# Kernel optimization log

Measured on AMD Instinct MI355X. Metric: run time of the kernel, lower is better.

The kernel has to match this reference:

```python
import jax, jax.numpy as jnp
import numpy as np


def _conv(x, w, b, stride=1, pad=0):
    # x: NCHW, w: OIHW
    y = jax.lax.conv_general_dilated(
        x, w, (stride, stride), [(pad, pad), (pad, pad)],
        dimension_numbers=('NCHW', 'OIHW', 'NCHW'))
    return y + b[None, :, None, None]


def _upsample2x(x):
    b, c, h, w = x.shape
    return jax.image.resize(x, (b, c, 2 * h, 2 * w), method='bilinear')


def setup_inputs() -> dict:
    key = jax.random.key(0)
    ks = jax.random.split(key, 16)
    B, H, W = 32, 256, 256
    K, D = 512, 64  # codebook_dim, latent_dim

    def kaiming(k, shape, fan_in):
        return jax.random.normal(k, shape, jnp.float32) * np.sqrt(2.0 / fan_in)

    inp = {
        'x': jax.random.uniform(ks[0], (B, 3, H, W), jnp.float32),
        'codebook': kaiming(ks[1], (K, D), D),
        'enc_w1': kaiming(ks[2], (64, 3, 3, 3), 3 * 9),
        'enc_b1': jnp.zeros((64,), jnp.float32),
        'enc_w2': kaiming(ks[3], (32, 64, 3, 3), 64 * 9),
        'enc_b2': jnp.zeros((32,), jnp.float32),
        'enc_w3': kaiming(ks[4], (D, 32, 1, 1), 32),
        'enc_b3': jnp.zeros((D,), jnp.float32),
        'dec_w1': kaiming(ks[5], (32, D, 1, 1), D),
        'dec_b1': jnp.zeros((32,), jnp.float32),
        'dec_w2': kaiming(ks[6], (64, 32, 3, 3), 32 * 9),
        'dec_b2': jnp.zeros((64,), jnp.float32),
        'dec_w3': kaiming(ks[7], (3, 64, 3, 3), 64 * 9),
        'dec_b3': jnp.zeros((3,), jnp.float32),
    }
    return inp


def reference(x, codebook, enc_w1, enc_b1, enc_w2, enc_b2, enc_w3, enc_b3,
              dec_w1, dec_b1, dec_w2, dec_b2, dec_w3, dec_b3):
    # ---- encoder ----
    h = jax.nn.relu(_conv(x, enc_w1, enc_b1, stride=2, pad=1))
    h = jax.nn.relu(_conv(h, enc_w2, enc_b2, stride=2, pad=1))
    latent = _conv(h, enc_w3, enc_b3)  # [B, D, h, w]

    b, c, hh, ww = latent.shape
    z = latent.transpose(0, 2, 3, 1).reshape(-1, c)  # [(b h w), D]

    # squared Euclidean distances; argmin identical to cdist argmin
    d2 = (jnp.sum(z * z, axis=1, keepdims=True)
          - 2.0 * z @ codebook.T
          + jnp.sum(codebook * codebook, axis=1)[None, :])
    indices = jnp.argmin(d2, axis=1)
    zq = codebook[indices]  # [(b h w), D]

    codebook_loss = jnp.mean((zq - jax.lax.stop_gradient(z)) ** 2)
    commitment_loss = jnp.mean((jax.lax.stop_gradient(zq) - z) ** 2)

    # straight-through estimator
    zq = z + jax.lax.stop_gradient(zq - z)
    zq = zq.reshape(b, hh, ww, c).transpose(0, 3, 1, 2)  # [B, D, h, w]

    # ---- decoder ----
    d = jax.nn.relu(_conv(zq, dec_w1, dec_b1))
    d = _upsample2x(d)
    d = jax.nn.relu(_conv(d, dec_w2, dec_b2, pad=1))
    d = _upsample2x(d)
    recon = _conv(d, dec_w3, dec_b3, pad=1)

    return codebook_loss, commitment_loss, recon
```

## Files before the change

kernel.cpp:

```cpp
#include <hip/hip_runtime.h>
#include <hip/hip_bf16.h>

static constexpr int Bn = 32;
static constexpr int Hin = 256, Win = 256;
static constexpr int C1 = 64, H1 = 128, W1 = 128;
static constexpr int C2 = 32, H2 = 64, W2 = 64;
static constexpr int Dd = 64;
static constexpr int Kc = 512;
static constexpr int ROWS = Bn * H2 * W2;

static constexpr int K2A_FLOATS = 64 * 32 * 36;
static constexpr int K2B_FLOATS = 3 * 64 * 36;
static constexpr int T1_FLOATS  = Kc * C2;
static constexpr int G_FLOATS   = Kc * 9 * 64 * 4;
static constexpr int FIX_FLOATS = 64 + ROWS + 2 * ROWS + K2A_FLOATS +
                                  K2B_FLOATS + T1_FLOATS + G_FLOATS + 64;
static constexpr int H1_PER_N = C1 * H1 * W1;
static constexpr int Z_PER_N  = H2 * W2 * Dd;
static constexpr int H2_PER_N = C2 * H2 * W2;

__global__ __launch_bounds__(256) void k_init(
    float* __restrict__ lossA, unsigned long long* __restrict__ pk)
{
  int i = blockIdx.x * 256 + threadIdx.x;
  if (i < 64) lossA[i] = 0.f;
  pk[i] = 0xFFFFFFFFFFFFFFFFull;
}

__global__ __launch_bounds__(256) void k_wtrans(
    const float* __restrict__ w, float* __restrict__ k2, int N)
{
  int i = blockIdx.x * 256 + threadIdx.x;
  if (i >= N) return;
  float W[3][3];
#pragma unroll
  for (int ty = 0; ty < 3; ++ty)
#pragma unroll
    for (int tx = 0; tx < 3; ++tx) W[ty][tx] = w[i * 9 + ty * 3 + tx];
  const float A[2][3][3] = {
      {{.75f, .25f, 0.f}, {.25f, .75f, 0.f}, {0.f, .75f, .25f}},
      {{.25f, .75f, 0.f}, {0.f, .75f, .25f}, {0.f, .25f, .75f}}};
#pragma unroll
  for (int py = 0; py < 2; ++py)
#pragma unroll
    for (int px = 0; px < 2; ++px)
#pragma unroll
      for (int a = 0; a < 3; ++a)
#pragma unroll
        for (int b = 0; b < 3; ++b) {
          float v = 0.f;
#pragma unroll
          for (int ty = 0; ty < 3; ++ty)
#pragma unroll
            for (int tx = 0; tx < 3; ++tx)
              v += W[ty][tx] * A[py][ty][a] * A[px][tx][b];
          k2[(size_t)i * 36 + (py * 2 + px) * 9 + a * 3 + b] = v;
        }
}

__global__ __launch_bounds__(256) void k_gtab1(
    const float* __restrict__ cb, const float* __restrict__ w1,
    const float* __restrict__ b1, float* __restrict__ T1)
{
  int g = blockIdx.x * 256 + threadIdx.x;
  int e = g >> 5, ci = g & 31;
  const float* c = cb + e * Dd;
  const float* wr = w1 + ci * Dd;
  float a = 0.f;
#pragma unroll
  for (int d = 0; d < Dd; ++d) a += c[d] * wr[d];
  a += b1[ci];
  T1[g] = a > 0.f ? a : 0.f;
}

__global__ __launch_bounds__(256) void k_gtab2(
    const float* __restrict__ k2a, const float* __restrict__ T1,
    float* __restrict__ G)
{
  int e = blockIdx.x;
  int tid = threadIdx.x;
  int co = tid >> 2, ph = tid & 3;
  __shared__ float sT[32];
  if (tid < 32) sT[tid] = T1[e * 32 + tid];
  __syncthreads();
  float acc[9];
#pragma unroll
  for (int ab = 0; ab < 9; ++ab) acc[ab] = 0.f;
  for (int ci = 0; ci < 32; ++ci) {
    float tv = sT[ci];
    const float* kp = k2a + (size_t)(co * 32 + ci) * 36 + ph * 9;
#pragma unroll
    for (int ab = 0; ab < 9; ++ab) acc[ab] += tv * kp[ab];
  }
#pragma unroll
  for (int ab = 0; ab < 9; ++ab)
    G[((size_t)e * 9 + ab) * 256 + tid] = acc[ab];
}

__global__ __launch_bounds__(256) void k_conv1(
    const float* __restrict__ x, const float* __restrict__ w,
    const float* __restrict__ b, float* __restrict__ h1, int n0)
{
  int bid = blockIdx.x;
  int xt = bid & 1, yt = (bid >> 1) & 15, cc = (bid >> 5) & 3, n = bid >> 7;
  int X0 = xt * 64, Y0 = yt * 8, co0 = cc * 16;
  __shared__ float sIn[3][17][130];
  int tid = threadIdx.x;
  for (int i = tid; i < 3 * 17 * 130; i += 256) {
    int ci = i / (17 * 130);
    int rr = (i / 130) % 17;
    int ccx = i % 130;
    int gy = 2 * Y0 - 1 + rr, gx = 2 * X0 - 1 + ccx;
    float v = 0.f;
    if (gy >= 0 && gy < Hin && gx >= 0 && gx < Win)
      v = x[(((size_t)(n0 + n) * 3 + ci) * Hin + gy) * Win + gx];
    sIn[ci][rr][ccx] = v;
  }
  __syncthreads();
  int lx = tid & 63, ys = tid >> 6;
  float acc[16][2];
#pragma unroll
  for (int c = 0; c < 16; ++c) { acc[c][0] = 0.f; acc[c][1] = 0.f; }
#pragma unroll
  for (int ci = 0; ci < 3; ++ci)
#pragma unroll
    for (int ky = 0; ky < 3; ++ky)
#pragma unroll
      for (int kx = 0; kx < 3; ++kx) {
        float u0 = sIn[ci][2 * ys + ky][2 * lx + kx];
        float u1 = sIn[ci][2 * ys + 8 + ky][2 * lx + kx];
#pragma unroll
        for (int c = 0; c < 16; ++c) {
          float wv = w[((co0 + c) * 3 + ci) * 9 + ky * 3 + kx];
          acc[c][0] += u0 * wv;
          acc[c][1] += u1 * wv;
        }
      }
#pragma unroll
  for (int c = 0; c < 16; ++c) {
    float bv = b[co0 + c];
    float v0 = acc[c][0] + bv; v0 = v0 > 0.f ? v0 : 0.f;
    float v1 = acc[c][1] + bv; v1 = v1 > 0.f ? v1 : 0.f;
    h1[((n * C1 + co0 + c) * H1 + Y0 + ys) * W1 + X0 + lx] = v0;
    h1[((n * C1 + co0 + c) * H1 + Y0 + ys + 4) * W1 + X0 + lx] = v1;
  }
}

__global__ __launch_bounds__(256) void k_conv2(
    const float* __restrict__ h1, const float* __restrict__ w,
    const float* __restrict__ b, float* __restrict__ h2)
{
  int bid = blockIdx.x;
  int yt = bid & 15, cg = (bid >> 4) & 3, n = bid >> 6;
  int Y0 = yt * 4, co0 = cg * 8;
  __shared__ float sIn[4][9][132];
  int tid = threadIdx.x;
  int lane = tid & 63, ys = tid >> 6;
  float acc[8];
#pragma unroll
  for (int c = 0; c < 8; ++c) acc[c] = 0.f;
  for (int cb0 = 0; cb0 < C1; cb0 += 4) {
    __syncthreads();
    {
      const float* src = h1 + ((size_t)(n * C1 + cb0 + ys)) * (H1 * W1);
      float va[9], vb[9], vt[9];
#pragma unroll
      for (int rr = 0; rr < 9; ++rr) {
        int gy = 2 * Y0 - 1 + rr;
        bool yok = (gy >= 0) & (gy < H1);
        const float* rowp = src + gy * W1;
        va[rr] = (yok && lane > 0) ? rowp[lane - 1] : 0.f;
        vb[rr] = yok ? rowp[lane + 63] : 0.f;
        vt[rr] = (yok && lane == 0) ? rowp[127] : 0.f;
      }
      float* dst = &sIn[ys][0][0];
#pragma unroll
      for (int rr = 0; rr < 9; ++rr) {
        dst[rr * 132 + lane] = va[rr];
        dst[rr * 132 + 64 + lane] = vb[rr];
        if (lane < 2) dst[rr * 132 + 128 + lane] = (lane == 0) ? vt[rr] : 0.f;
      }
    }
    __syncthreads();
#pragma unroll
    for (int ci = 0; ci < 4; ++ci)
#pragma unroll
      for (int ky = 0; ky < 3; ++ky)
#pragma unroll
        for (int kx = 0; kx < 3; ++kx) {
          float u0 = sIn[ci][2 * ys + ky][2 * lane + kx];
#pragma unroll
          for (int c = 0; c < 8; ++c) {
            float wv = w[((co0 + c) * C1 + cb0 + ci) * 9 + ky * 3 + kx];
            acc[c] += u0 * wv;
          }
        }
  }
#pragma unroll
  for (int c = 0; c < 8; ++c) {
    float bv = b[co0 + c];
    float v0 = acc[c] + bv; v0 = v0 > 0.f ? v0 : 0.f;
    h2[((n * C2 + co0 + c) * H2 + Y0 + ys) * W2 + lane] = v0;
  }
}

__global__ __launch_bounds__(256) void k_conv3z(
    const float* __restrict__ h2, const float* __restrict__ w,
    const float* __restrict__ b, float* __restrict__ z)
{
  int bid = blockIdx.x;
  int y = bid & 63, n = bid >> 6;
  __shared__ float sH[C2][64];
  __shared__ float sW[Dd * 33];
  int tid = threadIdx.x;
  for (int i = tid; i < C2 * 64; i += 256) {
    int ci = i >> 6, xx = i & 63;
    sH[ci][xx] = h2[((n * C2 + ci) * H2 + y) * W2 + xx];
  }
  for (int i = tid; i < Dd * C2; i += 256) {
    int d = i >> 5, ci = i & 31;
    sW[d * 33 + ci] = w[i];
  }
  __syncthreads();
  int dg = tid & 3, lx = tid >> 2;
  float acc[16];
#pragma unroll
  for (int j = 0; j < 16; ++j) acc[j] = 0.f;
  for (int ci = 0; ci < C2; ++ci) {
    float u = sH[ci][lx];
#pragma unroll
    for (int j = 0; j < 16; ++j)
      acc[j] += u * sW[(dg * 16 + j) * 33 + ci];
  }
  int row = (n * H2 + y) * W2 + lx;
#pragma unroll
  for (int j = 0; j < 16; ++j)
    z[row * Dd + dg * 16 + j] = acc[j] + b[dg * 16 + j];
}

__global__ __launch_bounds__(256, 1) void k_vq(
    const float* __restrict__ z, const float* __restrict__ cbf,
    unsigned long long* __restrict__ pk, int row0)
{
  __shared__ float c2s[128];
  int bid = blockIdx.x;
  int sp = bid & 3, rb = bid >> 2;
  int c0 = sp * 128;
  int tid = threadIdx.x;
  if (tid < 128) {
    const float* cr = cbf + (size_t)(c0 + tid) * Dd;
    float s = 0.f;
#pragma unroll
    for (int d = 0; d < Dd; ++d) { float v = cr[d]; s += v * v; }
    c2s[tid] = s;
  }
  __syncthreads();
  int r = rb * 256 + tid;
  const float4* zp = (const float4*)(z + (size_t)r * Dd);
  float4 z0 = zp[0],  z1 = zp[1],  z2 = zp[2],  z3 = zp[3];
  float4 z4 = zp[4],  z5 = zp[5],  z6 = zp[6],  z7 = zp[7];
  float4 z8 = zp[8],  z9 = zp[9],  z10 = zp[10], z11 = zp[11];
  float4 z12 = zp[12], z13 = zp[13], z14 = zp[14], z15 = zp[15];
  float best = 1e30f; int bidx = c0;
#pragma unroll 2
  for (int c = 0; c < 128; ++c) {
    const float* __restrict__ cr = cbf + (size_t)(c0 + c) * Dd;
    float d0 = 0.f, d1 = 0.f, d2a = 0.f, d3 = 0.f;
#define VQ_DOT(ZV, K)                       \
    d0 = __builtin_fmaf(ZV.x, cr[4*K+0], d0); \
    d1 = __builtin_fmaf(ZV.y, cr[4*K+1], d1); \
    d2a = __builtin_fmaf(ZV.z, cr[4*K+2], d2a); \
    d3 = __builtin_fmaf(ZV.w, cr[4*K+3], d3);
    VQ_DOT(z0, 0)  VQ_DOT(z1, 1)  VQ_DOT(z2, 2)  VQ_DOT(z3, 3)
    VQ_DOT(z4, 4)  VQ_DOT(z5, 5)  VQ_DOT(z6, 6)  VQ_DOT(z7, 7)
    VQ_DOT(z8, 8)  VQ_DOT(z9, 9)  VQ_DOT(z10, 10) VQ_DOT(z11, 11)
    VQ_DOT(z12, 12) VQ_DOT(z13, 13) VQ_DOT(z14, 14) VQ_DOT(z15, 15)
#undef VQ_DOT
    float dot = (d0 + d1) + (d2a + d3);
    float dist = c2s[c] - 2.f * dot;
    if (dist < best) { best = dist; bidx = c0 + c; }
  }
  unsigned int u = __float_as_uint(best);
  unsigned int key32 = (u & 0x80000000u) ? ~u : (u | 0x80000000u);
  unsigned long long key =
      ((unsigned long long)key32 << 32) | (unsigned int)bidx;
  atomicMin(&pk[row0 + r], key);
}

__global__ __launch_bounds__(256) void k_vqfin(
    const float* __restrict__ z, const float* __restrict__ cbf,
    const unsigned long long* __restrict__ pk, int* __restrict__ idx,
    float* __restrict__ lossA, int row0)
{
  int r = blockIdx.x * 256 + threadIdx.x;
  int gi = row0 + r;
  int bidx = (int)(pk[gi] & 0xFFFFFFFFull);
  idx[gi] = bidx;
  const float4* zp = (const float4*)(z + (size_t)r * Dd);
  const float4* cr = (const float4*)(cbf + (size_t)bidx * Dd);
  float ls = 0.f;
#pragma unroll
  for (int i = 0; i < 16; ++i) {
    float4 zv = zp[i], cv = cr[i];
    float e0 = zv.x - cv.x, e1 = zv.y - cv.y;
    float e2 = zv.z - cv.z, e3 = zv.w - cv.w;
    ls += e0 * e0 + e1 * e1 + e2 * e2 + e3 * e3;
  }
#pragma unroll
  for (int off = 32; off > 0; off >>= 1) ls += __shfl_down(ls, off);
  if ((threadIdx.x & 63) == 0) atomicAdd(lossA, ls);
}

__global__ void k_loss_final(const float* __restrict__ a, float* __restrict__ out)
{
  if (threadIdx.x == 0) {
    float l = a[0] / (float)(ROWS * Dd);
    out[0] = l;
    out[1] = l;
  }
}

__global__ __launch_bounds__(256) void k_upg(
    const int* __restrict__ idx, const float* __restrict__ G,
    const float* __restrict__ bias, float* __restrict__ O, int row0)
{
  int bid = blockIdx.x;
  int tx = bid & 3; bid >>= 2;
  int ty = bid & 3; bid >>= 2;
  int cog = bid & 7; bid >>= 3;
  int n = bid;
  int Y0 = ty * 16, X0 = tx * 16, co0 = cog * 8;
  __shared__ int sIdx[18 * 18];
  int tid = threadIdx.x;
  int base = row0 + (n << 12);
  for (int i = tid; i < 324; i += 256) {
    int r = i / 18, c = i % 18;
    int gy = Y0 - 1 + r; gy = gy < 0 ? 0 : (gy > 63 ? 63 : gy);
    int gx = X0 - 1 + c; gx = gx < 0 ? 0 : (gx > 63 ? 63 : gx);
    sIdx[i] = idx[base + gy * 64 + gx];
  }
  __syncthreads();
  int xx = tid & 15, yy = tid >> 4;
  float4 acc[8];
#pragma unroll
  for (int j = 0; j < 8; ++j) acc[j] = make_float4(0.f, 0.f, 0.f, 0.f);
#pragma unroll
  for (int a = 0; a < 3; ++a)
#pragma unroll
    for (int b = 0; b < 3; ++b) {
      int e = sIdx[(yy + a) * 18 + xx + b];
      const float4* gp =
          (const float4*)(G + ((size_t)(e * 9 + a * 3 + b) * 256) + co0 * 4);
#pragma unroll
      for (int j = 0; j < 8; ++j) {
        float4 gv = gp[j];
        acc[j].x += gv.x; acc[j].y += gv.y;
        acc[j].z += gv.z; acc[j].w += gv.w;
      }
    }
  int oy = 2 * (Y0 + yy), ox = 2 * (X0 + xx);
#pragma unroll
  for (int j = 0; j < 8; ++j) {
    int co = co0 + j;
    float bv = bias[co];
    float2 r0, r1;
    r0.x = acc[j].x + bv; r0.y = acc[j].y + bv;
    r1.x = acc[j].z + bv; r1.y = acc[j].w + bv;
    r0.x = r0.x > 0.f ? r0.x : 0.f; r0.y = r0.y > 0.f ? r0.y : 0.f;
    r1.x = r1.x > 0.f ? r1.x : 0.f; r1.y = r1.y > 0.f ? r1.y : 0.f;
    size_t o = ((size_t)(n * 64 + co) * 128 + oy) * 128 + ox;
    *(float2*)&O[o] = r0;
    *(float2*)&O[o + 128] = r1;
  }
}

__global__ __launch_bounds__(256) void k_border_a(
    const int* __restrict__ idx, const float* __restrict__ T1,
    const float* __restrict__ w2, const float* __restrict__ b2,
    float* __restrict__ d2, int row0)
{
  int bid = blockIdx.x;
  int ch = bid & 1; bid >>= 1;
  int side = bid & 3; bid >>= 2;
  int n = bid;
  bool hside = side < 2;
  int rbase = (side == 1) ? 62 : 0;
  int cbase = (side == 3) ? 62 : 0;
  __shared__ int sE[128];
  __shared__ float sD[32 * 128];
  int tid = threadIdx.x;
  if (tid < 128) {
    int yy, xx;
    if (hside) { yy = rbase + (tid >> 6); xx = tid & 63; }
    else       { yy = tid >> 1; xx = cbase + (tid & 1); }
    sE[tid] = idx[row0 + (n << 12) + yy * 64 + xx];
  }
  __syncthreads();
  for (int t = tid; t < 32 * 128; t += 256) {
    int ci = t >> 7, j = t & 127;
    sD[t] = T1[sE[j] * 32 + ci];
  }
  __syncthreads();
  int px = tid & 127, q = tid >> 7;
  int co0 = (ch * 2 + q) * 16;
  int u, v;
  if (side == 0)      { u = 0;   v = px; }
  else if (side == 1) { u = 127; v = px; }
  else if (side == 2) { u = px;  v = 0;   if (px == 0 || px == 127) return; }
  else                { u = px;  v = 127; if (px == 0 || px == 127) return; }
  float acc[16];
#pragma unroll
  for (int j = 0; j < 16; ++j) acc[j] = 0.f;
  for (int ci = 0; ci < 32; ++ci) {
    const float* P = sD + ci * 128;
    float u9[9];
#pragma unroll
    for (int dy = -1; dy <= 1; ++dy)
#pragma unroll
      for (int dx = -1; dx <= 1; ++dx) {
        int uy = u + dy, ux = v + dx;
        float val = 0.f;
        if (uy >= 0 && uy < 128 && ux >= 0 && ux < 128) {
          int ky0, ky1, kx0, kx1; float ay0, ax0;
          if (uy & 1) { ky0 = uy >> 1; ky1 = ky0 + 1; ay0 = .75f; }
          else        { ky1 = uy >> 1; ky0 = ky1 - 1; ay0 = .25f; }
          if (ux & 1) { kx0 = ux >> 1; kx1 = kx0 + 1; ax0 = .75f; }
          else        { kx1 = ux >> 1; kx0 = kx1 - 1; ax0 = .25f; }
          ky0 = ky0 < 0 ? 0 : (ky0 > 63 ? 63 : ky0);
          ky1 = ky1 < 0 ? 0 : (ky1 > 63 ? 63 : ky1);
          kx0 = kx0 < 0 ? 0 : (kx0 > 63 ? 63 : kx0);
          kx1 = kx1 < 0 ? 0 : (kx1 > 63 ? 63 : kx1);
          int i00, i01, i10, i11;
          if (hside) {
            i00 = (ky0 - rbase) * 64 + kx0; i01 = (ky0 - rbase) * 64 + kx1;
            i10 = (ky1 - rbase) * 64 + kx0; i11 = (ky1 - rbase) * 64 + kx1;
          } else {
            i00 = ky0 * 2 + (kx0 - cbase); i01 = ky0 * 2 + (kx1 - cbase);
            i10 = ky1 * 2 + (kx0 - cbase); i11 = ky1 * 2 + (kx1 - cbase);
          }
          float ay1 = 1.f - ay0, ax1 = 1.f - ax0;
          val = ay0 * (ax0 * P[i00] + ax1 * P[i01]) +
                ay1 * (ax0 * P[i10] + ax1 * P[i11]);
        }
        u9[(dy + 1) * 3 + (dx + 1)] = val;
      }
#pragma unroll
    for (int j = 0; j < 16; ++j) {
      const float* wp = w2 + ((size_t)((co0 + j) * 32 + ci)) * 9;
#pragma unroll
      for (int tp = 0; tp < 9; ++tp) acc[j] += u9[tp] * wp[tp];
    }
  }
#pragma unroll
  for (int j = 0; j < 16; ++j) {
    int co = co0 + j;
    float val = acc[j] + b2[co];
    val = val > 0.f ? val : 0.f;
    d2[((size_t)(n * 64 + co) * 128 + u) * 128 + v] = val;
  }
}

__global__ __launch_bounds__(128) void k_upconv2x_b(
    const float* __restrict__ I, const float* __restrict__ k2,
    const float* __restrict__ bias, float* __restrict__ O, int n0)
{
  constexpr int Hi = 128, Ci = 64, Co = 3;
  int bid = blockIdx.x;
  int tx = bid & 3; bid >>= 2;
  int ty = bid & 15; bid >>= 4;
  int n = bid;
  int Y0 = ty * 8, X0 = tx * 32;
  __shared__ float sI[4][10 * 35];
  int tid = threadIdx.x;
  int lx = tid & 15, ly = tid >> 4;
  float4 acc[3][2];
#pragma unroll
  for (int j = 0; j < 3; ++j)
#pragma unroll
    for (int py = 0; py < 2; ++py) acc[j][py] = make_float4(0.f, 0.f, 0.f, 0.f);
  for (int c0 = 0; c0 < Ci; c0 += 4) {
    __syncthreads();
    for (int i = tid; i < 4 * 10 * 34; i += 128) {
      int s = i / 340, r2 = i % 340;
      int rr = r2 / 34, cc2 = r2 % 34;
      int gy = Y0 - 1 + rr; gy = gy < 0 ? 0 : (gy > Hi - 1 ? Hi - 1 : gy);
      int gx = X0 - 1 + cc2; gx = gx < 0 ? 0 : (gx > Hi - 1 ? Hi - 1 : gx);
      sI[s][rr * 35 + cc2] = I[((size_t)n * Ci + c0 + s) * Hi * Hi + gy * Hi + gx];
    }
    __syncthreads();
#pragma unroll
    for (int s = 0; s < 4; ++s) {
      float t[3][4];
#pragma unroll
      for (int r = 0; r < 3; ++r)
#pragma unroll
        for (int c = 0; c < 4; ++c)
          t[r][c] = sI[s][(ly + r) * 35 + 2 * lx + c];
#pragma unroll
      for (int j = 0; j < 3; ++j) {
        const float* kj = k2 + ((size_t)j * Ci + c0 + s) * 36;
#pragma unroll
        for (int a = 0; a < 3; ++a)
#pragma unroll
          for (int b = 0; b < 3; ++b) {
            float w00 = kj[a * 3 + b];
            float w01 = kj[9 + a * 3 + b];
            float w10 = kj[18 + a * 3 + b];
            float w11 = kj[27 + a * 3 + b];
            float i0 = t[a][b];
            float i1 = t[a][b + 1];
            acc[j][0].x += i0 * w00;
            acc[j][0].y += i0 * w01;
            acc[j][0].z += i1 * w00;
            acc[j][0].w += i1 * w01;
            acc[j][1].x += i0 * w10;
            acc[j][1].y += i0 * w11;
            acc[j][1].z += i1 * w10;
            acc[j][1].w += i1 * w11;
          }
      }
    }
  }
  int ox = 2 * X0 + 4 * lx;
  int oy0 = 2 * (Y0 + ly);
#pragma unroll
  for (int j = 0; j < 3; ++j) {
    float bv = bias[j];
#pragma unroll
    for (int py = 0; py < 2; ++py) {
      float4 v = acc[j][py];
      v.x += bv; v.y += bv; v.z += bv; v.w += bv;
      size_t off = (((size_t)((n0 + n) * Co + j)) * 256 + oy0 + py) * 256 + ox;
      *(float4*)&O[off] = v;
    }
  }
}

__global__ __launch_bounds__(256) void k_border_b(
    const float* __restrict__ d2, const float* __restrict__ w3,
    const float* __restrict__ b3, float* __restrict__ O, int n0)
{
  int bid = blockIdx.x;
  int side = bid & 3; int n = bid >> 2;
  bool hside = side < 2;
  int rbase = (side == 1) ? 126 : 0;
  int cbase = (side == 3) ? 126 : 0;
  __shared__ float sD[32 * 256];
  int tid = threadIdx.x;
  int px = tid;
  int u, v;
  if (side == 0)      { u = 0;   v = px; }
  else if (side == 1) { u = 255; v = px; }
  else if (side == 2) { u = px;  v = 0; }
  else                { u = px;  v = 255; }
  bool active = hside || (px != 0 && px != 255);
  float a0 = 0.f, a1 = 0.f, a2 = 0.f;
  for (int half = 0; half < 2; ++half) {
    __syncthreads();
    int cib = half * 32;
    for (int t = tid; t < 32 * 256; t += 256) {
      int ci = t >> 8, j = t & 255;
      int yy, xx;
      if (hside) { yy = rbase + (j >> 7); xx = j & 127; }
      else       { yy = j >> 1; xx = cbase + (j & 1); }
      sD[t] = d2[(((size_t)n * 64 + cib + ci) * 128 + yy) * 128 + xx];
    }
    __syncthreads();
    if (active) {
      for (int ci = 0; ci < 32; ++ci) {
        const float* P = sD + ci * 256;
        float u9[9];
#pragma unroll
        for (int dy = -1; dy <= 1; ++dy)
#pragma unroll
          for (int dx = -1; dx <= 1; ++dx) {
            int uy = u + dy, ux = v + dx;
            float val = 0.f;
            if (uy >= 0 && uy < 256 && ux >= 0 && ux < 256) {
              int ky0, ky1, kx0, kx1; float ay0, ax0;
              if (uy & 1) { ky0 = uy >> 1; ky1 = ky0 + 1; ay0 = .75f; }
              else        { ky1 = uy >> 1; ky0 = ky1 - 1; ay0 = .25f; }
              if (ux & 1) { kx0 = ux >> 1; kx1 = kx0 + 1; ax0 = .75f; }
              else        { kx1 = ux >> 1; kx0 = kx1 - 1; ax0 = .25f; }
              ky0 = ky0 < 0 ? 0 : (ky0 > 127 ? 127 : ky0);
              ky1 = ky1 < 0 ? 0 : (ky1 > 127 ? 127 : ky1);
              kx0 = kx0 < 0 ? 0 : (kx0 > 127 ? 127 : kx0);
              kx1 = kx1 < 0 ? 0 : (kx1 > 127 ? 127 : kx1);
              int i00, i01, i10, i11;
              if (hside) {
                i00 = (ky0 - rbase) * 128 + kx0; i01 = (ky0 - rbase) * 128 + kx1;
                i10 = (ky1 - rbase) * 128 + kx0; i11 = (ky1 - rbase) * 128 + kx1;
              } else {
                i00 = ky0 * 2 + (kx0 - cbase); i01 = ky0 * 2 + (kx1 - cbase);
                i10 = ky1 * 2 + (kx0 - cbase); i11 = ky1 * 2 + (kx1 - cbase);
              }
              float ay1 = 1.f - ay0, ax1 = 1.f - ax0;
              val = ay0 * (ax0 * P[i00] + ax1 * P[i01]) +
                    ay1 * (ax0 * P[i10] + ax1 * P[i11]);
            }
            u9[(dy + 1) * 3 + (dx + 1)] = val;
          }
        const float* w0 = w3 + ((size_t)(0 * 64 + cib + ci)) * 9;
        const float* w1 = w3 + ((size_t)(1 * 64 + cib + ci)) * 9;
        const float* w2p = w3 + ((size_t)(2 * 64 + cib + ci)) * 9;
#pragma unroll
        for (int tp = 0; tp < 9; ++tp) {
          a0 += u9[tp] * w0[tp];
          a1 += u9[tp] * w1[tp];
          a2 += u9[tp] * w2p[tp];
        }
      }
    }
  }
  if (active) {
    size_t b = ((size_t)(n0 + n) * 3) * 65536 + (size_t)u * 256 + v;
    O[b] = a0 + b3[0];
    O[b + 65536] = a1 + b3[1];
    O[b + 131072] = a2 + b3[2];
  }
}

extern "C" void kernel_launch(void* const* d_in, const int* in_sizes, int n_in,
                              void* d_out, int out_size, void* d_ws, size_t ws_size,
                              hipStream_t stream)
{
  const float* x      = (const float*)d_in[0];
  const float* cb     = (const float*)d_in[1];
  const float* enc_w1 = (const float*)d_in[2];
  const float* enc_b1 = (const float*)d_in[3];
  const float* enc_w2 = (const float*)d_in[4];
  const float* enc_b2 = (const float*)d_in[5];
  const float* enc_w3 = (const float*)d_in[6];
  const float* enc_b3 = (const float*)d_in[7];
  const float* dec_w1 = (const float*)d_in[8];
  const float* dec_b1 = (const float*)d_in[9];
  const float* dec_w2 = (const float*)d_in[10];
  const float* dec_b2 = (const float*)d_in[11];
  const float* dec_w3 = (const float*)d_in[12];
  const float* dec_b3 = (const float*)d_in[13];

  float* ws = (float*)d_ws;
  float* lossA = ws;
  int* idx = (int*)(lossA + 64);
  unsigned long long* pk = (unsigned long long*)(idx + ROWS);
  float* k2a = (float*)(pk + ROWS);
  float* k2b = k2a + K2A_FLOATS;
  float* T1  = k2b + K2B_FLOATS;
  float* G   = T1 + T1_FLOATS;
  float* chunkbuf = G + G_FLOATS + 64;

  int CH = 1;
  for (int c = 32; c >= 1; c >>= 1) {
    size_t need = ((size_t)FIX_FLOATS + (size_t)(H1_PER_N + Z_PER_N + H2_PER_N) * c) * 4;
    if (need <= ws_size) { CH = c; break; }
  }
  float* h1 = chunkbuf;
  float* z  = h1 + (size_t)H1_PER_N * CH;
  float* h2 = z + (size_t)Z_PER_N * CH;

  k_init<<<ROWS / 256, 256, 0, stream>>>(lossA, pk);
  k_wtrans<<<(64 * 32 + 255) / 256, 256, 0, stream>>>(dec_w2, k2a, 64 * 32);
  k_wtrans<<<1, 256, 0, stream>>>(dec_w3, k2b, 3 * 64);
  k_gtab1<<<64, 256, 0, stream>>>(cb, dec_w1, dec_b1, T1);
  k_gtab2<<<Kc, 256, 0, stream>>>(k2a, T1, G);

  float* out = (float*)d_out;

  for (int n0 = 0; n0 < Bn; n0 += CH) {
    int row0 = n0 * H2 * W2;
    k_conv1<<<CH * 128, 256, 0, stream>>>(x, enc_w1, enc_b1, h1, n0);
    k_conv2<<<CH * 64, 256, 0, stream>>>(h1, enc_w2, enc_b2, h2);
    k_conv3z<<<CH * 64, 256, 0, stream>>>(h2, enc_w3, enc_b3, z);
    k_vq<<<CH * 16 * 4, 256, 0, stream>>>(z, cb, pk, row0);
    k_vqfin<<<CH * 16, 256, 0, stream>>>(z, cb, pk, idx, lossA, row0);
    k_upg<<<CH * 8 * 16, 256, 0, stream>>>(idx, G, dec_b2, h1, row0);
    k_border_a<<<CH * 4 * 2, 256, 0, stream>>>(idx, T1, dec_w2, dec_b2, h1, row0);
    k_upconv2x_b<<<CH * 64, 128, 0, stream>>>(h1, k2b, dec_b3, out + 2, n0);
    k_border_b<<<CH * 4, 256, 0, stream>>>(h1, dec_w3, dec_b3, out + 2, n0);
  }
  k_loss_final<<<1, 64, 0, stream>>>(lossA, out);
}
```

Before: 1.014 ms.

## Store conv1 output channels-last and rewrite conv2 to read NHWC directly

conv1 now writes h1 in NHWC layout with float4 stores. conv2 is rewritten to read float4 channel vectors straight from global memory, with no shared-memory staging, and uses a pre-transposed weight table with 16 output channels per thread. This removes the shared-memory tile loads, the barriers and the scattered weight indexing. The cost is uncoalesced strided global loads, because each lane reads a different pixel 256 bytes apart with stride 2. Half as many blocks are launched.

```diff
diff --git a/kernel.cpp b/kernel.cpp
--- a/kernel.cpp
+++ b/kernel.cpp
@@ -13,8 +13,10 @@
 static constexpr int K2B_FLOATS = 3 * 64 * 36;
 static constexpr int T1_FLOATS  = Kc * C2;
 static constexpr int G_FLOATS   = Kc * 9 * 64 * 4;
+static constexpr int WT2_FLOATS = 2 * 9 * 64 * 16;
 static constexpr int FIX_FLOATS = 64 + ROWS + 2 * ROWS + K2A_FLOATS +
-                                  K2B_FLOATS + T1_FLOATS + G_FLOATS + 64;
+                                  K2B_FLOATS + T1_FLOATS + G_FLOATS + 64 +
+                                  WT2_FLOATS;
 static constexpr int H1_PER_N = C1 * H1 * W1;
 static constexpr int Z_PER_N  = H2 * W2 * Dd;
 static constexpr int H2_PER_N = C2 * H2 * W2;
@@ -56,6 +58,21 @@
               v += W[ty][tx] * A[py][ty][a] * A[px][tx][b];
           k2[(size_t)i * 36 + (py * 2 + px) * 9 + a * 3 + b] = v;
         }
+}
+
+__global__ __launch_bounds__(256) void k_wt2(
+    const float* __restrict__ w2, float* __restrict__ wT)
+{
+  int i = blockIdx.x * 256 + threadIdx.x;
+  if (i >= WT2_FLOATS) return;
+  int j = i & 15;
+  int r = i >> 4;
+  int ci = r & 63;
+  int s = r >> 6;
+  int tap = s % 9;
+  int cg = s / 9;
+  int co = cg * 16 + j;
+  wT[i] = w2[((size_t)co * C1 + ci) * 9 + tap];
 }
 
 __global__ __launch_bounds__(256) void k_gtab1(
@@ -136,71 +153,74 @@
           acc[c][1] += u1 * wv;
         }
       }
-#pragma unroll
-  for (int c = 0; c < 16; ++c) {
-    float bv = b[co0 + c];
-    float v0 = acc[c][0] + bv; v0 = v0 > 0.f ? v0 : 0.f;
-    float v1 = acc[c][1] + bv; v1 = v1 > 0.f ? v1 : 0.f;
-    h1[((n * C1 + co0 + c) * H1 + Y0 + ys) * W1 + X0 + lx] = v0;
-    h1[((n * C1 + co0 + c) * H1 + Y0 + ys + 4) * W1 + X0 + lx] = v1;
+  size_t p0 = (((size_t)n * H1 + Y0 + ys) * W1 + X0 + lx) * C1 + co0;
+  size_t p1 = (((size_t)n * H1 + Y0 + ys + 4) * W1 + X0 + lx) * C1 + co0;
+#pragma unroll
+  for (int c = 0; c < 16; c += 4) {
+    float4 s0, s1;
+    float bv;
+    bv = b[co0 + c + 0];
+    s0.x = acc[c + 0][0] + bv; s1.x = acc[c + 0][1] + bv;
+    bv = b[co0 + c + 1];
+    s0.y = acc[c + 1][0] + bv; s1.y = acc[c + 1][1] + bv;
+    bv = b[co0 + c + 2];
+    s0.z = acc[c + 2][0] + bv; s1.z = acc[c + 2][1] + bv;
+    bv = b[co0 + c + 3];
+    s0.w = acc[c + 3][0] + bv; s1.w = acc[c + 3][1] + bv;
+    s0.x = s0.x > 0.f ? s0.x : 0.f; s0.y = s0.y > 0.f ? s0.y : 0.f;
+    s0.z = s0.z > 0.f ? s0.z : 0.f; s0.w = s0.w > 0.f ? s0.w : 0.f;
+    s1.x = s1.x > 0.f ? s1.x : 0.f; s1.y = s1.y > 0.f ? s1.y : 0.f;
+    s1.z = s1.z > 0.f ? s1.z : 0.f; s1.w = s1.w > 0.f ? s1.w : 0.f;
+    *(float4*)&h1[p0 + c] = s0;
+    *(float4*)&h1[p1 + c] = s1;
   }
 }
 
 __global__ __launch_bounds__(256) void k_conv2(
-    const float* __restrict__ h1, const float* __restrict__ w,
+    const float* __restrict__ h1n, const float* __restrict__ wT,
     const float* __restrict__ b, float* __restrict__ h2)
 {
   int bid = blockIdx.x;
-  int yt = bid & 15, cg = (bid >> 4) & 3, n = bid >> 6;
-  int Y0 = yt * 4, co0 = cg * 8;
-  __shared__ float sIn[4][9][132];
-  int tid = threadIdx.x;
-  int lane = tid & 63, ys = tid >> 6;
-  float acc[8];
-#pragma unroll
-  for (int c = 0; c < 8; ++c) acc[c] = 0.f;
-  for (int cb0 = 0; cb0 < C1; cb0 += 4) {
-    __syncthreads();
-    {
-      const float* src = h1 + ((size_t)(n * C1 + cb0 + ys)) * (H1 * W1);
-      float va[9], vb[9], vt[9];
-#pragma unroll
-      for (int rr = 0; rr < 9; ++rr) {
-        int gy = 2 * Y0 - 1 + rr;
-        bool yok = (gy >= 0) & (gy < H1);
-        const float* rowp = src + gy * W1;
-        va[rr] = (yok && lane > 0) ? rowp[lane - 1] : 0.f;
-        vb[rr] = yok ? rowp[lane + 63] : 0.f;
-        vt[rr] = (yok && lane == 0) ? rowp[127] : 0.f;
-      }
-      float* dst = &sIn[ys][0][0];
-#pragma unroll
-      for (int rr = 0; rr < 9; ++rr) {
-        dst[rr * 132 + lane] = va[rr];
-        dst[rr * 132 + 64 + lane] = vb[rr];
-        if (lane < 2) dst[rr * 132 + 128 + lane] = (lane == 0) ? vt[rr] : 0.f;
+  int yt = bid & 15, cg = (bid >> 4) & 1, n = bid >> 5;
+  int tid = threadIdx.x;
+  int x = tid & 63, y = yt * 4 + (tid >> 6);
+  int co0 = cg * 16;
+  float acc[16];
+#pragma unroll
+  for (int j = 0; j < 16; ++j) acc[j] = 0.f;
+  const float* wg = wT + (size_t)cg * (9 * 64 * 16);
+#pragma unroll 1
+  for (int ky = 0; ky < 3; ++ky) {
+    int gy = 2 * y - 1 + ky;
+    if (gy < 0 || gy >= H1) continue;
+    const float* rowbase = h1n + ((size_t)n * H1 + gy) * W1 * C1;
+#pragma unroll 1
+    for (int kx = 0; kx < 3; ++kx) {
+      int gx = 2 * x - 1 + kx;
+      bool ok = (gx >= 0);
+      const float4* ip =
+          (const float4*)(rowbase + (size_t)(ok ? gx : 0) * C1);
+      const float* wp = wg + (ky * 3 + kx) * (64 * 16);
+#pragma unroll 4
+      for (int c4 = 0; c4 < 16; ++c4) {
+        float4 u = ip[c4];
+        if (!ok) { u.x = 0.f; u.y = 0.f; u.z = 0.f; u.w = 0.f; }
+        const float* w4 = wp + c4 * 64;
+#pragma unroll
+        for (int j = 0; j < 16; ++j) {
+          acc[j] = __builtin_fmaf(u.x, w4[j], acc[j]);
+          acc[j] = __builtin_fmaf(u.y, w4[16 + j], acc[j]);
+          acc[j] = __builtin_fmaf(u.z, w4[32 + j], acc[j]);
+          acc[j] = __builtin_fmaf(u.w, w4[48 + j], acc[j]);
+        }
       }
     }
-    __syncthreads();
-#pragma unroll
-    for (int ci = 0; ci < 4; ++ci)
-#pragma unroll
-      for (int ky = 0; ky < 3; ++ky)
-#pragma unroll
-        for (int kx = 0; kx < 3; ++kx) {
-          float u0 = sIn[ci][2 * ys + ky][2 * lane + kx];
-#pragma unroll
-          for (int c = 0; c < 8; ++c) {
-            float wv = w[((co0 + c) * C1 + cb0 + ci) * 9 + ky * 3 + kx];
-            acc[c] += u0 * wv;
-          }
-        }
-  }
-#pragma unroll
-  for (int c = 0; c < 8; ++c) {
-    float bv = b[co0 + c];
-    float v0 = acc[c] + bv; v0 = v0 > 0.f ? v0 : 0.f;
-    h2[((n * C2 + co0 + c) * H2 + Y0 + ys) * W2 + lane] = v0;
+  }
+#pragma unroll
+  for (int j = 0; j < 16; ++j) {
+    float v = acc[j] + b[co0 + j];
+    v = v > 0.f ? v : 0.f;
+    h2[(((size_t)n * C2 + co0 + j) * H2 + y) * W2 + x] = v;
   }
 }
 
@@ -647,7 +667,8 @@
   float* k2b = k2a + K2A_FLOATS;
   float* T1  = k2b + K2B_FLOATS;
   float* G   = T1 + T1_FLOATS;
-  float* chunkbuf = G + G_FLOATS + 64;
+  float* wT2 = G + G_FLOATS + 64;
+  float* chunkbuf = wT2 + WT2_FLOATS;
 
   int CH = 1;
   for (int c = 32; c >= 1; c >>= 1) {
@@ -661,6 +682,7 @@
   k_init<<<ROWS / 256, 256, 0, stream>>>(lossA, pk);
   k_wtrans<<<(64 * 32 + 255) / 256, 256, 0, stream>>>(dec_w2, k2a, 64 * 32);
   k_wtrans<<<1, 256, 0, stream>>>(dec_w3, k2b, 3 * 64);
+  k_wt2<<<(WT2_FLOATS + 255) / 256, 256, 0, stream>>>(enc_w2, wT2);
   k_gtab1<<<64, 256, 0, stream>>>(cb, dec_w1, dec_b1, T1);
   k_gtab2<<<Kc, 256, 0, stream>>>(k2a, T1, G);
 
@@ -669,7 +691,7 @@
   for (int n0 = 0; n0 < Bn; n0 += CH) {
     int row0 = n0 * H2 * W2;
     k_conv1<<<CH * 128, 256, 0, stream>>>(x, enc_w1, enc_b1, h1, n0);
-    k_conv2<<<CH * 64, 256, 0, stream>>>(h1, enc_w2, enc_b2, h2);
+    k_conv2<<<CH * 32, 256, 0, stream>>>(h1, wT2, enc_b2, h2);
     k_conv3z<<<CH * 64, 256, 0, stream>>>(h2, enc_w3, enc_b3, z);
     k_vq<<<CH * 16 * 4, 256, 0, stream>>>(z, cb, pk, row0);
     k_vqfin<<<CH * 16, 256, 0, stream>>>(z, cb, pk, idx, lossA, row0);
```

Result: faster. 923.5 us (-8.9%).
